# Kernel optimization log

Hardware: AMD Instinct MI355X
Metric: run time of the kernel (lower is better)

## Reference

```python
import jax, jax.numpy as jnp
import numpy as np

N_NODES = 50000
N_EDGES = 800000
IN_DIM = 128
HID = 128
OUT_DIM = 1
N_LAYERS = 3
NUM_GRAPHS = 500
LN_EPS = 1e-5


def setup_inputs() -> dict:
    key = jax.random.key(0)
    ks = jax.random.split(key, 16)
    x = jax.random.normal(ks[0], (N_NODES, IN_DIM), dtype=jnp.float32)
    edge_index = jax.random.randint(ks[1], (2, N_EDGES), 0, N_NODES, dtype=jnp.int32)
    batch = jnp.sort(jax.random.randint(ks[2], (N_NODES,), 0, NUM_GRAPHS, dtype=jnp.int32))
    s_in = 1.0 / np.sqrt(IN_DIM)
    s_h = 1.0 / np.sqrt(HID)
    W_in = jax.random.normal(ks[3], (HID, IN_DIM), jnp.float32) * s_in
    b_in = jnp.zeros((HID,), jnp.float32)
    Wc = jax.random.normal(ks[4], (N_LAYERS, HID, HID), jnp.float32) * s_h
    bc = jnp.zeros((N_LAYERS, HID), jnp.float32)
    gamma = jnp.ones((N_LAYERS, HID), jnp.float32)
    beta = jnp.zeros((N_LAYERS, HID), jnp.float32)
    W1 = jax.random.normal(ks[5], (HID // 2, HID), jnp.float32) * s_h
    b1 = jnp.zeros((HID // 2,), jnp.float32)
    W2 = jax.random.normal(ks[6], (OUT_DIM, HID // 2), jnp.float32) * (1.0 / np.sqrt(HID // 2))
    b2 = jnp.zeros((OUT_DIM,), jnp.float32)
    return dict(x=x, edge_index=edge_index, batch=batch, W_in=W_in, b_in=b_in,
                Wc=Wc, bc=bc, gamma=gamma, beta=beta, W1=W1, b1=b1, W2=W2, b2=b2)


def _layernorm(h, g, b):
    mu = jnp.mean(h, axis=-1, keepdims=True)
    var = jnp.mean(jnp.square(h - mu), axis=-1, keepdims=True)
    return (h - mu) * jax.lax.rsqrt(var + LN_EPS) * g + b


def reference(x, edge_index, batch, W_in, b_in, Wc, bc, gamma, beta, W1, b1, W2, b2):
    n = x.shape[0]
    src, dst = edge_index[0], edge_index[1]
    # GCN symmetric normalization with self-loops: deg_i = 1 + in-degree
    deg = jax.ops.segment_sum(jnp.ones_like(src, dtype=x.dtype), dst, num_segments=n) + 1.0
    dinv = jax.lax.rsqrt(deg)                       # [N]
    enorm = (dinv[src] * dinv[dst])[:, None]        # [E,1]
    self_norm = (dinv * dinv)[:, None]              # [N,1]

    h = x @ W_in.T + b_in                           # input projection [N,H]
    for l in range(N_LAYERS):
        res = h
        hw = h @ Wc[l].T                            # GCNConv linear (no bias)
        agg = jax.ops.segment_sum(hw[src] * enorm, dst, num_segments=n)
        agg = agg + hw * self_norm + bc[l]          # self-loop term + conv bias
        h = jax.nn.relu(_layernorm(agg, gamma[l], beta[l])) + res  # dropout is identity in eval

    # global_mean_pool
    counts = jax.ops.segment_sum(jnp.ones((n,), x.dtype), batch, num_segments=NUM_GRAPHS)
    pooled = jax.ops.segment_sum(h, batch, num_segments=NUM_GRAPHS) / jnp.maximum(counts, 1.0)[:, None]

    out = jax.nn.relu(pooled @ W1.T + b1) @ W2.T + b2
    return out
```

## Files before the change

kernel.cpp:

```cpp
#include <hip/hip_runtime.h>
#include <hip/hip_bf16.h>

#define HIDDIM 128
#define CAP 4096

typedef short bf16x8 __attribute__((ext_vector_type(8)));
typedef float f32x4 __attribute__((ext_vector_type(4)));

__device__ inline unsigned short f2bf(float f) {
    unsigned u = __float_as_uint(f);
    unsigned r = (u + 0x7fffu + ((u >> 16) & 1u)) >> 16;
    return (unsigned short)r;
}
__device__ inline float bf2f(unsigned short s) {
    return __uint_as_float(((unsigned)s) << 16);
}

__global__ __launch_bounds__(256) void init_gcursor(int* __restrict__ gcursor, int nbuck) {
    int b = blockIdx.x * 256 + threadIdx.x;
    if (b < nbuck) gcursor[b] = b * CAP;
}

__global__ __launch_bounds__(256) void bucket_scatter(const int* __restrict__ ei, int E,
                                                      int* __restrict__ gcursor,
                                                      unsigned* __restrict__ ebuf, int nbuck) {
    __shared__ int lcount[512];
    __shared__ int lbase[512];
    int t = threadIdx.x;
    int cb = blockIdx.x * 2048;
    lcount[t] = 0;
    lcount[t + 256] = 0;
    __syncthreads();

    int bkt[8];
    int lpos[8];
    unsigned pk[8];
#pragma unroll
    for (int j = 0; j < 8; ++j) {
        int e = cb + j * 256 + t;
        if (e < E) {
            int s_ = ei[e];
            int d_ = ei[E + e];
            bkt[j] = d_ >> 7;
            pk[j] = ((unsigned)s_ << 7) | (unsigned)(d_ & 127);
            lpos[j] = atomicAdd(&lcount[bkt[j]], 1);
        } else {
            bkt[j] = -1;
            lpos[j] = 0;
            pk[j] = 0;
        }
    }
    __syncthreads();
    for (int bb = t; bb < nbuck; bb += 256) {
        int c = lcount[bb];
        lbase[bb] = c ? atomicAdd(&gcursor[bb], c) : 0;
    }
    __syncthreads();
#pragma unroll
    for (int j = 0; j < 8; ++j) {
        if (bkt[j] >= 0) {
            unsigned idx = (unsigned)lbase[bkt[j]] + (unsigned)lpos[j];
            if (idx < (unsigned)(bkt[j] + 1) * CAP)
                ebuf[idx] = pk[j];
        }
    }
}

__global__ __launch_bounds__(256) void bucket_scan(const int* __restrict__ gcursor, int nbuck,
                                                   int* __restrict__ bptr,
                                                   int* __restrict__ rowptr, int N) {
    int t = threadIdx.x;
    int lane = t & 63, wave = t >> 6;
    int i0 = 2 * t, i1 = 2 * t + 1;
    int c0 = (i0 < nbuck) ? gcursor[i0] - i0 * CAP : 0;
    int c1 = (i1 < nbuck) ? gcursor[i1] - i1 * CAP : 0;
    int s = c0 + c1;
    int inc = s;
#pragma unroll
    for (int off = 1; off < 64; off <<= 1) {
        int u = __shfl_up(inc, off);
        if (lane >= off) inc += u;
    }
    __shared__ int wtot[4];
    if (lane == 63) wtot[wave] = inc;
    __syncthreads();
    int wbase = 0;
    for (int w = 0; w < wave; ++w) wbase += wtot[w];
    inc += wbase;
    int excl = inc - s;
    if (i0 < nbuck) bptr[i0] = excl;
    if (i1 < nbuck) bptr[i1] = excl + c0;
    if (t == 255) {
        int total = wtot[0] + wtot[1] + wtot[2] + wtot[3];
        bptr[nbuck] = total;
        rowptr[N] = total;
    }
}

__global__ __launch_bounds__(256) void csr_build(const unsigned* __restrict__ ebuf,
                                                 const int* __restrict__ bptr, int N,
                                                 int* __restrict__ rowptr,
                                                 int* __restrict__ csr_src,
                                                 float* __restrict__ dinv) {
    __shared__ int hist[128];
    __shared__ int excl[128];
    __shared__ int cur[128];
    int b = blockIdx.x;
    int t = threadIdx.x;
    int node0 = b << 7;
    int e0 = bptr[b], e1 = bptr[b + 1];
    int cnt = e1 - e0;
    if (t < 128) hist[t] = 0;
    __syncthreads();
    const unsigned* slab = ebuf + (size_t)b * CAP;
    for (int k = t; k < cnt; k += 256) atomicAdd(&hist[slab[k] & 127], 1);
    __syncthreads();
    if (t < 128) excl[t] = hist[t];
    __syncthreads();
    for (int off = 1; off < 128; off <<= 1) {
        int v = (t < 128 && t >= off) ? excl[t - off] : 0;
        __syncthreads();
        if (t < 128) excl[t] += v;
        __syncthreads();
    }
    if (t < 128) {
        int ex = excl[t] - hist[t];
        excl[t] = ex;
        cur[t] = ex;
    }
    __syncthreads();
    int nn = N - node0;
    if (nn > 128) nn = 128;
    if (t < nn) {
        rowptr[node0 + t] = e0 + excl[t];
        dinv[node0 + t] = 1.0f / sqrtf((float)hist[t] + 1.0f);
    }
    for (int k = t; k < cnt; k += 256) {
        unsigned p = slab[k];
        int dl = p & 127;
        int pos = atomicAdd(&cur[dl], 1);
        csr_src[e0 + pos] = (int)(p >> 7);
    }
}

__global__ __launch_bounds__(256) void graph_ptr_kernel(const int* __restrict__ batch, int n,
                                                        int G, int* __restrict__ gp) {
    int i = blockIdx.x * 256 + threadIdx.x;
    if (i >= n) return;
    int bi = batch[i];
    if (i == 0) {
        for (int g = 0; g <= bi; ++g) gp[g] = 0;
    } else {
        int bp = batch[i - 1];
        for (int g = bp + 1; g <= bi; ++g) gp[g] = i;
    }
    if (i == n - 1) {
        for (int g = bi + 1; g <= G; ++g) gp[g] = n;
    }
}

__global__ __launch_bounds__(256) void prep_wfrag(const float* __restrict__ Win,
                                                  const float* __restrict__ Wc,
                                                  unsigned short* __restrict__ Wfrag) {
    int gid = blockIdx.x * 256 + threadIdx.x;
    if (gid >= 4 * 16384) return;
    int m = gid >> 14;
    int r = gid & 16383;
    int t = r >> 11;
    int kk = (r >> 9) & 3;
    int lane = (r >> 3) & 63;
    int j = r & 7;
    int kg = lane >> 4, oc = lane & 15;
    int o = t * 16 + oc;
    int k = kk * 32 + kg * 8 + j;
    const float* src = (m == 0) ? Win : (Wc + (m - 1) * 16384);
    float w = src[o * 128 + k];
    unsigned short hi = f2bf(w);
    unsigned short lo = f2bf(w - bf2f(hi));
    Wfrag[m * 32768 + r] = hi;
    Wfrag[m * 32768 + 16384 + r] = lo;
}

__global__ __launch_bounds__(256) void gemm_mfma(const float* __restrict__ A,
                                                 const unsigned short* __restrict__ Wfrag,
                                                 const float* __restrict__ bias,
                                                 const float* __restrict__ scale,
                                                 void* __restrict__ Cout, int n, int use_bias,
                                                 int use_scale, int out_bf16) {
    __shared__ unsigned short sB[32768];
    int tid = threadIdx.x;
    int wave = tid >> 6;
    int lane = tid & 63;
    int wbase = blockIdx.x * 64 + wave * 16;

    {
        const float4* src = (const float4*)Wfrag;
        float4* dst = (float4*)sB;
#pragma unroll
        for (int i = 0; i < 16; ++i) dst[tid + i * 256] = src[tid + i * 256];
    }
    __syncthreads();

    f32x4 acc[8];
#pragma unroll
    for (int t = 0; t < 8; ++t) acc[t] = (f32x4){0.f, 0.f, 0.f, 0.f};

    int arow = wbase + (lane & 15);
    int kg8 = (lane >> 4) * 8;

#pragma unroll
    for (int kk = 0; kk < 4; ++kk) {
        float4 v0 = {0.f, 0.f, 0.f, 0.f}, v1 = {0.f, 0.f, 0.f, 0.f};
        if (arow < n) {
            const float* ap = A + (size_t)arow * 128 + kk * 32 + kg8;
            v0 = *(const float4*)(ap);
            v1 = *(const float4*)(ap + 4);
        }
        float fs[8] = {v0.x, v0.y, v0.z, v0.w, v1.x, v1.y, v1.z, v1.w};
        bf16x8 ahi, alo;
#pragma unroll
        for (int j = 0; j < 8; ++j) {
            unsigned short h = f2bf(fs[j]);
            ahi[j] = (short)h;
            alo[j] = (short)f2bf(fs[j] - bf2f(h));
        }
#pragma unroll
        for (int t = 0; t < 8; ++t) {
            int boff = ((t * 4 + kk) * 64 + lane) * 8;
            bf16x8 bhi = *(const bf16x8*)(sB + boff);
            bf16x8 blo = *(const bf16x8*)(sB + 16384 + boff);
            acc[t] = __builtin_amdgcn_mfma_f32_16x16x32_bf16(ahi, bhi, acc[t], 0, 0, 0);
            acc[t] = __builtin_amdgcn_mfma_f32_16x16x32_bf16(ahi, blo, acc[t], 0, 0, 0);
            acc[t] = __builtin_amdgcn_mfma_f32_16x16x32_bf16(alo, bhi, acc[t], 0, 0, 0);
        }
    }

    int colbase = lane & 15;
    int rquad = (lane >> 4) * 4;
    float bvs[8];
#pragma unroll
    for (int t = 0; t < 8; ++t) bvs[t] = use_bias ? bias[t * 16 + colbase] : 0.0f;
#pragma unroll
    for (int r = 0; r < 4; ++r) {
        int gr = wbase + rquad + r;
        if (gr >= n) continue;
        float s = use_scale ? scale[gr] : 1.0f;
        if (out_bf16) {
            unsigned short* crow = (unsigned short*)Cout + (size_t)gr * 128;
#pragma unroll
            for (int t = 0; t < 8; ++t) crow[t * 16 + colbase] = f2bf((acc[t][r] + bvs[t]) * s);
        } else {
            float* crow = (float*)Cout + (size_t)gr * 128;
#pragma unroll
            for (int t = 0; t < 8; ++t) crow[t * 16 + colbase] = (acc[t][r] + bvs[t]) * s;
        }
    }
}

__global__ __launch_bounds__(256) void gather_ln(const unsigned short* __restrict__ hws,
                                                 float* __restrict__ h,
                                                 const int* __restrict__ rowptr,
                                                 const int* __restrict__ csr_src,
                                                 const float* __restrict__ dinv,
                                                 const float* __restrict__ bc,
                                                 const float* __restrict__ gamma,
                                                 const float* __restrict__ beta, int n) {
    int wid = (blockIdx.x * 256 + threadIdx.x) >> 6;
    int lane = threadIdx.x & 63;
    if (wid >= n) return;
    int i = wid;
    float di = dinv[i];
    int e0 = rowptr[i], e1 = rowptr[i + 1];
    int c0 = lane * 2;
    const unsigned short* hb = hws + c0;

    ushort2 r0 = *(const ushort2*)(hb + (size_t)i * HIDDIM);
    float sx = bf2f(r0.x), sy = bf2f(r0.y);
    int e = e0;
    for (; e + 8 <= e1; e += 8) {
        int i0 = csr_src[e + 0], i1 = csr_src[e + 1], i2 = csr_src[e + 2], i3 = csr_src[e + 3];
        int i4 = csr_src[e + 4], i5 = csr_src[e + 5], i6 = csr_src[e + 6], i7 = csr_src[e + 7];
        ushort2 v0 = *(const ushort2*)(hb + (size_t)i0 * HIDDIM);
        ushort2 v1 = *(const ushort2*)(hb + (size_t)i1 * HIDDIM);
        ushort2 v2 = *(const ushort2*)(hb + (size_t)i2 * HIDDIM);
        ushort2 v3 = *(const ushort2*)(hb + (size_t)i3 * HIDDIM);
        ushort2 v4 = *(const ushort2*)(hb + (size_t)i4 * HIDDIM);
        ushort2 v5 = *(const ushort2*)(hb + (size_t)i5 * HIDDIM);
        ushort2 v6 = *(const ushort2*)(hb + (size_t)i6 * HIDDIM);
        ushort2 v7 = *(const ushort2*)(hb + (size_t)i7 * HIDDIM);
        sx += bf2f(v0.x); sy += bf2f(v0.y);  sx += bf2f(v1.x); sy += bf2f(v1.y);
        sx += bf2f(v2.x); sy += bf2f(v2.y);  sx += bf2f(v3.x); sy += bf2f(v3.y);
        sx += bf2f(v4.x); sy += bf2f(v4.y);  sx += bf2f(v5.x); sy += bf2f(v5.y);
        sx += bf2f(v6.x); sy += bf2f(v6.y);  sx += bf2f(v7.x); sy += bf2f(v7.y);
    }
    if (e + 4 <= e1) {
        int i0 = csr_src[e + 0], i1 = csr_src[e + 1], i2 = csr_src[e + 2], i3 = csr_src[e + 3];
        ushort2 v0 = *(const ushort2*)(hb + (size_t)i0 * HIDDIM);
        ushort2 v1 = *(const ushort2*)(hb + (size_t)i1 * HIDDIM);
        ushort2 v2 = *(const ushort2*)(hb + (size_t)i2 * HIDDIM);
        ushort2 v3 = *(const ushort2*)(hb + (size_t)i3 * HIDDIM);
        sx += bf2f(v0.x); sy += bf2f(v0.y);  sx += bf2f(v1.x); sy += bf2f(v1.y);
        sx += bf2f(v2.x); sy += bf2f(v2.y);  sx += bf2f(v3.x); sy += bf2f(v3.y);
        e += 4;
    }
    for (; e < e1; ++e) {
        int sc = csr_src[e];
        ushort2 v = *(const ushort2*)(hb + (size_t)sc * HIDDIM);
        sx += bf2f(v.x); sy += bf2f(v.y);
    }
    float2 bcv = *(const float2*)(bc + c0);
    float vx = di * sx + bcv.x;
    float vy = di * sy + bcv.y;

    float s1 = vx + vy, s2 = vx * vx + vy * vy;
#pragma unroll
    for (int off = 32; off; off >>= 1) {
        s1 += __shfl_xor(s1, off);
        s2 += __shfl_xor(s2, off);
    }
    float mu = s1 * (1.0f / 128.0f);
    float var = s2 * (1.0f / 128.0f) - mu * mu;
    float rs = 1.0f / sqrtf(var + 1e-5f);

    float2 gm = *(const float2*)(gamma + c0);
    float2 bt = *(const float2*)(beta + c0);
    float yx = fmaxf((vx - mu) * rs * gm.x + bt.x, 0.0f);
    float yy = fmaxf((vy - mu) * rs * gm.y + bt.y, 0.0f);

    float2 hv = *(float2*)(h + (size_t)i * HIDDIM + c0);
    hv.x += yx; hv.y += yy;
    *(float2*)(h + (size_t)i * HIDDIM + c0) = hv;
}

__global__ __launch_bounds__(128) void pool_mlp_kernel(const float* __restrict__ h,
                                                       const int* __restrict__ gp,
                                                       const float* __restrict__ W1,
                                                       const float* __restrict__ b1,
                                                       const float* __restrict__ W2,
                                                       const float* __restrict__ b2,
                                                       float* __restrict__ out, int G) {
    __shared__ float sp[128];
    int g = blockIdx.x;
    if (g >= G) return;
    int t = threadIdx.x;
    int s = gp[g], e = gp[g + 1];
    float acc = 0.0f;
    for (int i = s; i < e; ++i) acc += h[(size_t)i * HIDDIM + t];
    float cnt = fmaxf((float)(e - s), 1.0f);
    sp[t] = acc / cnt;
    __syncthreads();
    if (t < 64) {
        const float* wr = W1 + t * HIDDIM;
        float a = 0.0f;
#pragma unroll 8
        for (int k = 0; k < HIDDIM; k += 4) {
            float4 p = *(const float4*)(sp + k);
            float4 w = *(const float4*)(wr + k);
            a += p.x * w.x + p.y * w.y + p.z * w.z + p.w * w.w;
        }
        float h1 = fmaxf(a + b1[t], 0.0f);
        float c = h1 * W2[t];
#pragma unroll
        for (int off = 32; off; off >>= 1) c += __shfl_xor(c, off);
        if (t == 0) out[g] = c + b2[0];
    }
}

extern "C" void kernel_launch(void* const* d_in, const int* in_sizes, int n_in,
                              void* d_out, int out_size, void* d_ws, size_t ws_size,
                              hipStream_t stream) {
    const float* x      = (const float*)d_in[0];
    const int*   ei     = (const int*)d_in[1];
    const int*   batch  = (const int*)d_in[2];
    const float* W_in   = (const float*)d_in[3];
    const float* b_in   = (const float*)d_in[4];
    const float* Wc     = (const float*)d_in[5];
    const float* bc     = (const float*)d_in[6];
    const float* gamma  = (const float*)d_in[7];
    const float* beta   = (const float*)d_in[8];
    const float* W1     = (const float*)d_in[9];
    const float* b1     = (const float*)d_in[10];
    const float* W2     = (const float*)d_in[11];
    const float* b2     = (const float*)d_in[12];
    float* out = (float*)d_out;

    const int N = in_sizes[2];
    const int E = in_sizes[1] / 2;
    const int G = out_size;
    const int NBUCK = (N + 127) >> 7;

    char* ws = (char*)d_ws;
    size_t off = 0;
    auto alloc = [&](size_t bytes) {
        size_t o = off;
        off = (off + bytes + 255) & ~(size_t)255;
        return o;
    };
    int*      rowptr  = (int*)(ws + alloc((size_t)(N + 1) * 4));
    int*      csr_src = (int*)(ws + alloc((size_t)E * 4));
    float*    dinv    = (float*)(ws + alloc((size_t)N * 4));
    unsigned* ebuf    = (unsigned*)(ws + alloc((size_t)NBUCK * CAP * 4));
    int*      gcursor = (int*)(ws + alloc((size_t)NBUCK * 4));
    int*      bptr    = (int*)(ws + alloc((size_t)(NBUCK + 1) * 4));
    unsigned short* Wfrag = (unsigned short*)(ws + alloc((size_t)4 * 32768 * 2));
    float*    h       = (float*)(ws + alloc((size_t)N * 128 * 4));
    unsigned short* hws = (unsigned short*)(ws + alloc((size_t)N * 128 * 2));
    int*      gp      = (int*)(ws + alloc((size_t)(G + 1) * 4));
    (void)ws_size; (void)n_in;

    init_gcursor<<<(NBUCK + 255) / 256, 256, 0, stream>>>(gcursor, NBUCK);
    bucket_scatter<<<(E + 2047) / 2048, 256, 0, stream>>>(ei, E, gcursor, ebuf, NBUCK);
    bucket_scan<<<1, 256, 0, stream>>>(gcursor, NBUCK, bptr, rowptr, N);
    csr_build<<<NBUCK, 256, 0, stream>>>(ebuf, bptr, N, rowptr, csr_src, dinv);
    graph_ptr_kernel<<<(N + 255) / 256, 256, 0, stream>>>(batch, N, G, gp);
    prep_wfrag<<<(4 * 16384 + 255) / 256, 256, 0, stream>>>(W_in, Wc, Wfrag);

    int mblocks = (N + 63) / 64;
    gemm_mfma<<<mblocks, 256, 0, stream>>>(x, Wfrag, b_in, nullptr, h, N, 1, 0, 0);

    for (int l = 0; l < 3; ++l) {
        gemm_mfma<<<mblocks, 256, 0, stream>>>(h, Wfrag + (1 + l) * 32768, nullptr, dinv,
                                               hws, N, 0, 1, 1);
        gather_ln<<<(N + 3) / 4, 256, 0, stream>>>(hws, h, rowptr, csr_src, dinv,
                                                   bc + l * 128, gamma + l * 128,
                                                   beta + l * 128, N);
    }

    pool_mlp_kernel<<<G, 128, 0, stream>>>(h, gp, W1, b1, W2, b2, out, G);
}
```

Measured before the change: 332.0 us.

## Merge small preprocessing kernels, double GEMM block size, unroll pool accumulation

The cursor init, graph-pointer build and weight-fragment prep kernels are folded into one launch that dispatches on block index, cutting two kernel launches. The MFMA GEMM now runs 512-thread blocks covering 128 rows, so each block amortizes the 64KB shared-memory weight load over twice as many rows. The pooling loop uses two accumulators to expose more memory-level parallelism. Larger blocks reduce occupancy granularity and halve the block count.

```diff
diff --git a/kernel.cpp b/kernel.cpp
--- a/kernel.cpp
+++ b/kernel.cpp
@@ -16,153 +16,37 @@
     return __uint_as_float(((unsigned)s) << 16);
 }
 
-__global__ __launch_bounds__(256) void init_gcursor(int* __restrict__ gcursor, int nbuck) {
-    int b = blockIdx.x * 256 + threadIdx.x;
-    if (b < nbuck) gcursor[b] = b * CAP;
-}
-
-__global__ __launch_bounds__(256) void bucket_scatter(const int* __restrict__ ei, int E,
-                                                      int* __restrict__ gcursor,
-                                                      unsigned* __restrict__ ebuf, int nbuck) {
-    __shared__ int lcount[512];
-    __shared__ int lbase[512];
-    int t = threadIdx.x;
-    int cb = blockIdx.x * 2048;
-    lcount[t] = 0;
-    lcount[t + 256] = 0;
-    __syncthreads();
-
-    int bkt[8];
-    int lpos[8];
-    unsigned pk[8];
-#pragma unroll
-    for (int j = 0; j < 8; ++j) {
-        int e = cb + j * 256 + t;
-        if (e < E) {
-            int s_ = ei[e];
-            int d_ = ei[E + e];
-            bkt[j] = d_ >> 7;
-            pk[j] = ((unsigned)s_ << 7) | (unsigned)(d_ & 127);
-            lpos[j] = atomicAdd(&lcount[bkt[j]], 1);
+__global__ __launch_bounds__(256) void preproc_misc(int* __restrict__ gcursor, int nbuck,
+                                                    const int* __restrict__ batch, int n, int G,
+                                                    int* __restrict__ gp,
+                                                    const float* __restrict__ Win,
+                                                    const float* __restrict__ Wc,
+                                                    unsigned short* __restrict__ Wfrag,
+                                                    int nbgp) {
+    int bx = blockIdx.x;
+    if (bx < 2) {
+        int b = bx * 256 + threadIdx.x;
+        if (b < nbuck) gcursor[b] = b * CAP;
+        return;
+    }
+    bx -= 2;
+    if (bx < nbgp) {
+        int i = bx * 256 + threadIdx.x;
+        if (i >= n) return;
+        int bi = batch[i];
+        if (i == 0) {
+            for (int g = 0; g <= bi; ++g) gp[g] = 0;
         } else {
-            bkt[j] = -1;
-            lpos[j] = 0;
-            pk[j] = 0;
-        }
-    }
-    __syncthreads();
-    for (int bb = t; bb < nbuck; bb += 256) {
-        int c = lcount[bb];
-        lbase[bb] = c ? atomicAdd(&gcursor[bb], c) : 0;
-    }
-    __syncthreads();
-#pragma unroll
-    for (int j = 0; j < 8; ++j) {
-        if (bkt[j] >= 0) {
-            unsigned idx = (unsigned)lbase[bkt[j]] + (unsigned)lpos[j];
-            if (idx < (unsigned)(bkt[j] + 1) * CAP)
-                ebuf[idx] = pk[j];
-        }
-    }
-}
-
-__global__ __launch_bounds__(256) void bucket_scan(const int* __restrict__ gcursor, int nbuck,
-                                                   int* __restrict__ bptr,
-                                                   int* __restrict__ rowptr, int N) {
-    int t = threadIdx.x;
-    int lane = t & 63, wave = t >> 6;
-    int i0 = 2 * t, i1 = 2 * t + 1;
-    int c0 = (i0 < nbuck) ? gcursor[i0] - i0 * CAP : 0;
-    int c1 = (i1 < nbuck) ? gcursor[i1] - i1 * CAP : 0;
-    int s = c0 + c1;
-    int inc = s;
-#pragma unroll
-    for (int off = 1; off < 64; off <<= 1) {
-        int u = __shfl_up(inc, off);
-        if (lane >= off) inc += u;
-    }
-    __shared__ int wtot[4];
-    if (lane == 63) wtot[wave] = inc;
-    __syncthreads();
-    int wbase = 0;
-    for (int w = 0; w < wave; ++w) wbase += wtot[w];
-    inc += wbase;
-    int excl = inc - s;
-    if (i0 < nbuck) bptr[i0] = excl;
-    if (i1 < nbuck) bptr[i1] = excl + c0;
-    if (t == 255) {
-        int total = wtot[0] + wtot[1] + wtot[2] + wtot[3];
-        bptr[nbuck] = total;
-        rowptr[N] = total;
-    }
-}
-
-__global__ __launch_bounds__(256) void csr_build(const unsigned* __restrict__ ebuf,
-                                                 const int* __restrict__ bptr, int N,
-                                                 int* __restrict__ rowptr,
-                                                 int* __restrict__ csr_src,
-                                                 float* __restrict__ dinv) {
-    __shared__ int hist[128];
-    __shared__ int excl[128];
-    __shared__ int cur[128];
-    int b = blockIdx.x;
-    int t = threadIdx.x;
-    int node0 = b << 7;
-    int e0 = bptr[b], e1 = bptr[b + 1];
-    int cnt = e1 - e0;
-    if (t < 128) hist[t] = 0;
-    __syncthreads();
-    const unsigned* slab = ebuf + (size_t)b * CAP;
-    for (int k = t; k < cnt; k += 256) atomicAdd(&hist[slab[k] & 127], 1);
-    __syncthreads();
-    if (t < 128) excl[t] = hist[t];
-    __syncthreads();
-    for (int off = 1; off < 128; off <<= 1) {
-        int v = (t < 128 && t >= off) ? excl[t - off] : 0;
-        __syncthreads();
-        if (t < 128) excl[t] += v;
-        __syncthreads();
-    }
-    if (t < 128) {
-        int ex = excl[t] - hist[t];
-        excl[t] = ex;
-        cur[t] = ex;
-    }
-    __syncthreads();
-    int nn = N - node0;
-    if (nn > 128) nn = 128;
-    if (t < nn) {
-        rowptr[node0 + t] = e0 + excl[t];
-        dinv[node0 + t] = 1.0f / sqrtf((float)hist[t] + 1.0f);
-    }
-    for (int k = t; k < cnt; k += 256) {
-        unsigned p = slab[k];
-        int dl = p & 127;
-        int pos = atomicAdd(&cur[dl], 1);
-        csr_src[e0 + pos] = (int)(p >> 7);
-    }
-}
-
-__global__ __launch_bounds__(256) void graph_ptr_kernel(const int* __restrict__ batch, int n,
-                                                        int G, int* __restrict__ gp) {
-    int i = blockIdx.x * 256 + threadIdx.x;
-    if (i >= n) return;
-    int bi = batch[i];
-    if (i == 0) {
-        for (int g = 0; g <= bi; ++g) gp[g] = 0;
-    } else {
-        int bp = batch[i - 1];
-        for (int g = bp + 1; g <= bi; ++g) gp[g] = i;
-    }
-    if (i == n - 1) {
-        for (int g = bi + 1; g <= G; ++g) gp[g] = n;
-    }
-}
-
-__global__ __launch_bounds__(256) void prep_wfrag(const float* __restrict__ Win,
-                                                  const float* __restrict__ Wc,
-                                                  unsigned short* __restrict__ Wfrag) {
-    int gid = blockIdx.x * 256 + threadIdx.x;
+            int bp = batch[i - 1];
+            for (int g = bp + 1; g <= bi; ++g) gp[g] = i;
+        }
+        if (i == n - 1) {
+            for (int g = bi + 1; g <= G; ++g) gp[g] = n;
+        }
+        return;
+    }
+    bx -= nbgp;
+    int gid = bx * 256 + threadIdx.x;
     if (gid >= 4 * 16384) return;
     int m = gid >> 14;
     int r = gid & 16383;
@@ -181,7 +65,129 @@
     Wfrag[m * 32768 + 16384 + r] = lo;
 }
 
-__global__ __launch_bounds__(256) void gemm_mfma(const float* __restrict__ A,
+__global__ __launch_bounds__(256) void bucket_scatter(const int* __restrict__ ei, int E,
+                                                      int* __restrict__ gcursor,
+                                                      unsigned* __restrict__ ebuf, int nbuck) {
+    __shared__ int lcount[512];
+    __shared__ int lbase[512];
+    int t = threadIdx.x;
+    int cb = blockIdx.x * 2048;
+    lcount[t] = 0;
+    lcount[t + 256] = 0;
+    __syncthreads();
+
+    int bkt[8];
+    int lpos[8];
+    unsigned pk[8];
+#pragma unroll
+    for (int j = 0; j < 8; ++j) {
+        int e = cb + j * 256 + t;
+        if (e < E) {
+            int s_ = ei[e];
+            int d_ = ei[E + e];
+            bkt[j] = d_ >> 7;
+            pk[j] = ((unsigned)s_ << 7) | (unsigned)(d_ & 127);
+            lpos[j] = atomicAdd(&lcount[bkt[j]], 1);
+        } else {
+            bkt[j] = -1;
+            lpos[j] = 0;
+            pk[j] = 0;
+        }
+    }
+    __syncthreads();
+    for (int bb = t; bb < nbuck; bb += 256) {
+        int c = lcount[bb];
+        lbase[bb] = c ? atomicAdd(&gcursor[bb], c) : 0;
+    }
+    __syncthreads();
+#pragma unroll
+    for (int j = 0; j < 8; ++j) {
+        if (bkt[j] >= 0) {
+            unsigned idx = (unsigned)lbase[bkt[j]] + (unsigned)lpos[j];
+            if (idx < (unsigned)(bkt[j] + 1) * CAP)
+                ebuf[idx] = pk[j];
+        }
+    }
+}
+
+__global__ __launch_bounds__(256) void bucket_scan(const int* __restrict__ gcursor, int nbuck,
+                                                   int* __restrict__ bptr,
+                                                   int* __restrict__ rowptr, int N) {
+    int t = threadIdx.x;
+    int lane = t & 63, wave = t >> 6;
+    int i0 = 2 * t, i1 = 2 * t + 1;
+    int c0 = (i0 < nbuck) ? gcursor[i0] - i0 * CAP : 0;
+    int c1 = (i1 < nbuck) ? gcursor[i1] - i1 * CAP : 0;
+    int s = c0 + c1;
+    int inc = s;
+#pragma unroll
+    for (int off = 1; off < 64; off <<= 1) {
+        int u = __shfl_up(inc, off);
+        if (lane >= off) inc += u;
+    }
+    __shared__ int wtot[4];
+    if (lane == 63) wtot[wave] = inc;
+    __syncthreads();
+    int wbase = 0;
+    for (int w = 0; w < wave; ++w) wbase += wtot[w];
+    inc += wbase;
+    int excl = inc - s;
+    if (i0 < nbuck) bptr[i0] = excl;
+    if (i1 < nbuck) bptr[i1] = excl + c0;
+    if (t == 255) {
+        int total = wtot[0] + wtot[1] + wtot[2] + wtot[3];
+        bptr[nbuck] = total;
+        rowptr[N] = total;
+    }
+}
+
+__global__ __launch_bounds__(256) void csr_build(const unsigned* __restrict__ ebuf,
+                                                 const int* __restrict__ bptr, int N,
+                                                 int* __restrict__ rowptr,
+                                                 int* __restrict__ csr_src,
+                                                 float* __restrict__ dinv) {
+    __shared__ int hist[128];
+    __shared__ int excl[128];
+    __shared__ int cur[128];
+    int b = blockIdx.x;
+    int t = threadIdx.x;
+    int node0 = b << 7;
+    int e0 = bptr[b], e1 = bptr[b + 1];
+    int cnt = e1 - e0;
+    if (t < 128) hist[t] = 0;
+    __syncthreads();
+    const unsigned* slab = ebuf + (size_t)b * CAP;
+    for (int k = t; k < cnt; k += 256) atomicAdd(&hist[slab[k] & 127], 1);
+    __syncthreads();
+    if (t < 128) excl[t] = hist[t];
+    __syncthreads();
+    for (int off = 1; off < 128; off <<= 1) {
+        int v = (t < 128 && t >= off) ? excl[t - off] : 0;
+        __syncthreads();
+        if (t < 128) excl[t] += v;
+        __syncthreads();
+    }
+    if (t < 128) {
+        int ex = excl[t] - hist[t];
+        excl[t] = ex;
+        cur[t] = ex;
+    }
+    __syncthreads();
+    int nn = N - node0;
+    if (nn > 128) nn = 128;
+    if (t < nn) {
+        rowptr[node0 + t] = e0 + excl[t];
+        dinv[node0 + t] = 1.0f / sqrtf((float)hist[t] + 1.0f);
+    }
+    for (int k = t; k < cnt; k += 256) {
+        unsigned p = slab[k];
+        int dl = p & 127;
+        int pos = atomicAdd(&cur[dl], 1);
+        csr_src[e0 + pos] = (int)(p >> 7);
+    }
+}
+
+__global__ __launch_bounds__(512) void gemm_mfma(const float* __restrict__ A,
                                                  const unsigned short* __restrict__ Wfrag,
                                                  const float* __restrict__ bias,
                                                  const float* __restrict__ scale,
@@ -191,13 +197,13 @@
     int tid = threadIdx.x;
     int wave = tid >> 6;
     int lane = tid & 63;
-    int wbase = blockIdx.x * 64 + wave * 16;
+    int wbase = blockIdx.x * 128 + wave * 16;
 
     {
         const float4* src = (const float4*)Wfrag;
         float4* dst = (float4*)sB;
 #pragma unroll
-        for (int i = 0; i < 16; ++i) dst[tid + i * 256] = src[tid + i * 256];
+        for (int i = 0; i < 8; ++i) dst[tid + i * 512] = src[tid + i * 512];
     }
     __syncthreads();
 
@@ -344,10 +350,15 @@
     if (g >= G) return;
     int t = threadIdx.x;
     int s = gp[g], e = gp[g + 1];
-    float acc = 0.0f;
-    for (int i = s; i < e; ++i) acc += h[(size_t)i * HIDDIM + t];
+    float a0 = 0.0f, a1 = 0.0f;
+    int i = s;
+    for (; i + 2 <= e; i += 2) {
+        a0 += h[(size_t)i * HIDDIM + t];
+        a1 += h[(size_t)(i + 1) * HIDDIM + t];
+    }
+    if (i < e) a0 += h[(size_t)i * HIDDIM + t];
     float cnt = fmaxf((float)(e - s), 1.0f);
-    sp[t] = acc / cnt;
+    sp[t] = (a0 + a1) / cnt;
     __syncthreads();
     if (t < 64) {
         const float* wr = W1 + t * HIDDIM;
@@ -408,18 +419,19 @@
     int*      gp      = (int*)(ws + alloc((size_t)(G + 1) * 4));
     (void)ws_size; (void)n_in;
 
-    init_gcursor<<<(NBUCK + 255) / 256, 256, 0, stream>>>(gcursor, NBUCK);
+    const int NBGP = (N + 255) / 256;
+    const int NBPW = (4 * 16384 + 255) / 256;
+    preproc_misc<<<2 + NBGP + NBPW, 256, 0, stream>>>(gcursor, NBUCK, batch, N, G, gp,
+                                                      W_in, Wc, Wfrag, NBGP);
     bucket_scatter<<<(E + 2047) / 2048, 256, 0, stream>>>(ei, E, gcursor, ebuf, NBUCK);
     bucket_scan<<<1, 256, 0, stream>>>(gcursor, NBUCK, bptr, rowptr, N);
     csr_build<<<NBUCK, 256, 0, stream>>>(ebuf, bptr, N, rowptr, csr_src, dinv);
-    graph_ptr_kernel<<<(N + 255) / 256, 256, 0, stream>>>(batch, N, G, gp);
-    prep_wfrag<<<(4 * 16384 + 255) / 256, 256, 0, stream>>>(W_in, Wc, Wfrag);
-
-    int mblocks = (N + 63) / 64;
-    gemm_mfma<<<mblocks, 256, 0, stream>>>(x, Wfrag, b_in, nullptr, h, N, 1, 0, 0);
+
+    int mblocks = (N + 127) / 128;
+    gemm_mfma<<<mblocks, 512, 0, stream>>>(x, Wfrag, b_in, nullptr, h, N, 1, 0, 0);
 
     for (int l = 0; l < 3; ++l) {
-        gemm_mfma<<<mblocks, 256, 0, stream>>>(h, Wfrag + (1 + l) * 32768, nullptr, dinv,
+        gemm_mfma<<<mblocks, 512, 0, stream>>>(h, Wfrag + (1 + l) * 32768, nullptr, dinv,
                                                hws, N, 0, 1, 1);
         gather_ln<<<(N + 3) / 4, 256, 0, stream>>>(hws, h, rowptr, csr_src, dinv,
                                                    bc + l * 128, gamma + l * 128,
```

Measured after the change: 298.1 us. 1.11x faster.
